# Kernel optimization log

Measured on AMD Instinct MI355X. Metric: run time of the kernel, lower is better.

The kernel has to match this reference:

```python
import jax, jax.numpy as jnp
import numpy as np

PI = float(np.pi)

def setup_inputs() -> dict:
    key = jax.random.key(0)
    k1, k2 = jax.random.split(key)
    B, S, NUM_CHARS, P = 8, 8192, 95, 8
    char_idx = jax.random.randint(k1, (B, S), 0, NUM_CHARS, dtype=jnp.int32)
    positions = jnp.arange(S, dtype=jnp.int32)
    W = jax.random.normal(k2, (NUM_CHARS, P), dtype=jnp.float32)
    return {"char_idx": char_idx, "positions": positions, "W": W}

def reference(char_idx, positions, W):
    """Vectorized PhysicalTokenizer.encode (learnable Phase 2, eval mode).
    char_idx: [B,S] int, already offset by ascii_start; W: [num_chars,8].
    Returns quaternion tensor [B, S, embed_dim, 4].
    """
    embed_dim = 128
    params = W[char_idx]                                  # [B,S,8] gather
    omega = params[..., 0:1] * 2.0                        # [B,S,1]
    A1, A2, A3 = params[..., 1:2], params[..., 2:3], params[..., 3:4]
    beta = params[..., 4:5]
    gamma = jax.nn.sigmoid(params[..., 5:6])
    phi = params[..., 6:7] * PI
    j = jnp.arange(embed_dim, dtype=jnp.float32)          # [D]
    # spectral wave synthesis, fused elementwise over [B,S,D]
    wave = (A1 * jnp.sin(omega * j + phi)
            + A2 * jnp.sin(2.0 * omega * j + 2.0 * phi)
            + A3 * jnp.sin(3.0 * omega * j + 3.0 * phi)) * jnp.exp(-gamma * j)
    pos_phase = jnp.sin(positions.astype(jnp.float32) * (0.1 * PI))  # [S]
    wave = wave + beta * j * pos_phase[None, :, None]     # [B,S,D]
    psi0 = wave
    psi1 = jnp.roll(wave, shift=1, axis=-1)
    psi2 = jnp.sin(wave)
    psi3 = jnp.cos(wave)
    return jnp.stack([psi0, psi1, psi2, psi3], axis=-1)   # [B,S,D,4]
```

## Files before the change

### kernel.cpp

```cpp
#include <hip/hip_runtime.h>

#define PI_F 3.14159265358979323846f

constexpr int ED = 128;
constexpr int ROWS_PER_BLOCK = 2;

__global__ __launch_bounds__(256) void ptok_kernel(
    const int* __restrict__ char_idx,
    const int* __restrict__ positions,
    const float* __restrict__ W,
    float* __restrict__ out,
    int S)
{
    const int local_row = threadIdx.x >> 7;
    const int j = threadIdx.x & (ED - 1);
    const int row = blockIdx.x * ROWS_PER_BLOCK + local_row;
    const int s = row & (S - 1);

    const int c = char_idx[row];
    const float* p = W + c * 8;
    const float omega = p[0] * 2.0f;
    const float A1 = p[1], A2 = p[2], A3 = p[3];
    const float beta = p[4];
    const float gamma = 1.0f / (1.0f + __expf(-p[5]));
    const float phi = p[6] * PI_F;

    const float fj = (float)j;
    const float arg1 = omega * fj + phi;
    const float arg2 = 2.0f * omega * fj + 2.0f * phi;
    const float arg3 = 3.0f * omega * fj + 3.0f * phi;
    const float env = __expf(-gamma * fj);
    float w = (A1 * __sinf(arg1) + A2 * __sinf(arg2) + A3 * __sinf(arg3)) * env;

    const float pos_phase = __sinf((float)positions[s] * (0.1f * PI_F));
    w += beta * fj * pos_phase;

    __shared__ float lds[ROWS_PER_BLOCK][ED];
    lds[local_row][j] = w;
    __syncthreads();
    const float wprev = lds[local_row][(j + ED - 1) & (ED - 1)];

    float4 o;
    o.x = w;
    o.y = wprev;
    o.z = __sinf(w);
    o.w = __cosf(w);
    reinterpret_cast<float4*>(out)[(size_t)row * ED + j] = o;
}

extern "C" void kernel_launch(void* const* d_in, const int* in_sizes, int n_in,
                              void* d_out, int out_size, void* d_ws, size_t ws_size,
                              hipStream_t stream) {
    const int* char_idx  = (const int*)d_in[0];
    const int* positions = (const int*)d_in[1];
    const float* W       = (const float*)d_in[2];
    float* out = (float*)d_out;

    const int nrows = in_sizes[0];
    const int S = in_sizes[1];

    const int grid = nrows / ROWS_PER_BLOCK;
    ptok_kernel<<<grid, 256, 0, stream>>>(char_idx, positions, W, out, S);
}
```

Measured before the change: 28.01 us.

## Map one wavefront per row with shuffle-based roll and trig identities

Each 64-lane wavefront now handles a full 128-element row, two elements per lane. The roll uses cross-lane shuffles instead of LDS plus a block barrier. sin(2a) and sin(3a) come from multiple-angle identities on one sin/cos pair instead of three separate sin calls, and the W row is read with two float4 loads. This trims transcendental work and removes synchronisation, but the kernel is mostly bound by output stores and the identities may change rounding slightly.

```diff
diff --git a/kernel.cpp b/kernel.cpp
--- a/kernel.cpp
+++ b/kernel.cpp
@@ -3,7 +3,7 @@
 #define PI_F 3.14159265358979323846f
 
 constexpr int ED = 128;
-constexpr int ROWS_PER_BLOCK = 2;
+constexpr int ROWS_PER_BLOCK = 4;
 
 __global__ __launch_bounds__(256) void ptok_kernel(
     const int* __restrict__ char_idx,
@@ -12,40 +12,47 @@
     float* __restrict__ out,
     int S)
 {
-    const int local_row = threadIdx.x >> 7;
-    const int j = threadIdx.x & (ED - 1);
-    const int row = blockIdx.x * ROWS_PER_BLOCK + local_row;
+    const int lane = threadIdx.x & 63;
+    const int wv = threadIdx.x >> 6;
+    const int row = blockIdx.x * ROWS_PER_BLOCK + wv;
     const int s = row & (S - 1);
 
     const int c = char_idx[row];
-    const float* p = W + c * 8;
-    const float omega = p[0] * 2.0f;
-    const float A1 = p[1], A2 = p[2], A3 = p[3];
-    const float beta = p[4];
-    const float gamma = 1.0f / (1.0f + __expf(-p[5]));
-    const float phi = p[6] * PI_F;
-
-    const float fj = (float)j;
-    const float arg1 = omega * fj + phi;
-    const float arg2 = 2.0f * omega * fj + 2.0f * phi;
-    const float arg3 = 3.0f * omega * fj + 3.0f * phi;
-    const float env = __expf(-gamma * fj);
-    float w = (A1 * __sinf(arg1) + A2 * __sinf(arg2) + A3 * __sinf(arg3)) * env;
+    const float4 p0 = reinterpret_cast<const float4*>(W + c * 8)[0];
+    const float4 p1 = reinterpret_cast<const float4*>(W + c * 8)[1];
+    const float omega = p0.x * 2.0f;
+    const float A1 = p0.y, A2 = p0.z, A3 = p0.w;
+    const float beta = p1.x;
+    const float gamma = 1.0f / (1.0f + __expf(-p1.y));
+    const float phi = p1.z * PI_F;
 
     const float pos_phase = __sinf((float)positions[s] * (0.1f * PI_F));
-    w += beta * fj * pos_phase;
 
-    __shared__ float lds[ROWS_PER_BLOCK][ED];
-    lds[local_row][j] = w;
-    __syncthreads();
-    const float wprev = lds[local_row][(j + ED - 1) & (ED - 1)];
+    float w01[2];
+    #pragma unroll
+    for (int k = 0; k < 2; ++k) {
+        const float fj = (float)(lane + 64 * k);
+        const float a = omega * fj + phi;
+        const float sa = __sinf(a);
+        const float ca = __cosf(a);
+        const float wave = (A1 * sa + A2 * (2.0f * sa * ca)
+                            + A3 * sa * (3.0f - 4.0f * sa * sa))
+                           * __expf(-gamma * fj);
+        w01[k] = wave + beta * fj * pos_phase;
+    }
 
-    float4 o;
-    o.x = w;
-    o.y = wprev;
-    o.z = __sinf(w);
-    o.w = __cosf(w);
-    reinterpret_cast<float4*>(out)[(size_t)row * ED + j] = o;
+    const int lm1 = (lane + 63) & 63;
+    const float u0 = __shfl(w01[0], lm1, 64);
+    const float u1 = __shfl(w01[1], lm1, 64);
+    const float prev0 = (lane == 0) ? u1 : u0;
+    const float prev1 = (lane == 0) ? u0 : u1;
+
+    float4* orow = reinterpret_cast<float4*>(out) + (size_t)row * ED;
+    float4 o0, o1;
+    o0.x = w01[0]; o0.y = prev0; o0.z = __sinf(w01[0]); o0.w = __cosf(w01[0]);
+    o1.x = w01[1]; o1.y = prev1; o1.z = __sinf(w01[1]); o1.w = __cosf(w01[1]);
+    orow[lane] = o0;
+    orow[64 + lane] = o1;
 }
 
 extern "C" void kernel_launch(void* const* d_in, const int* in_sizes, int n_in,
```

New measurement: 26.40 us. 1.06x faster.
